# Performance work log

Measured on AMD Instinct MI355X. Metric: run time of the kernel, lower is better.

Reference implementation:

```python
import jax, jax.numpy as jnp
import numpy as np

B, T, E, H = 2, 4096, 1024, 16
D = E // H  # head dim = 64

def setup_inputs() -> dict:
    key = jax.random.key(0)
    ks = jax.random.split(key, 5)
    x = jax.random.normal(ks[0], (B, T, E), dtype=jnp.float32)
    # torch Linear(n_embed, 3*n_embed): y = x @ W.T + b ; we store W already transposed as (E, 3E)
    w_qkv = jax.random.normal(ks[1], (E, 3 * E), dtype=jnp.float32) * (1.0 / np.sqrt(E))
    b_qkv = jax.random.normal(ks[2], (3 * E,), dtype=jnp.float32) * 0.02
    w_out = jax.random.normal(ks[3], (E, E), dtype=jnp.float32) * (1.0 / np.sqrt(E))
    b_out = jax.random.normal(ks[4], (E,), dtype=jnp.float32) * 0.02
    return {"x": x, "w_qkv": w_qkv, "b_qkv": b_qkv, "w_out": w_out, "b_out": b_out}

def reference(x, w_qkv, b_qkv, w_out, b_out):
    b, t, e = x.shape
    qkv = x @ w_qkv + b_qkv                      # (B,T,3E)
    # matches torch: view(B,T,H,3D) then chunk(3, dim=-1)
    qkv = qkv.reshape(b, t, H, 3 * D)
    q, k, v = jnp.split(qkv, 3, axis=-1)          # each (B,T,H,D)
    q = q.transpose(0, 2, 1, 3)                   # (B,H,T,D)
    k = k.transpose(0, 2, 1, 3)
    v = v.transpose(0, 2, 1, 3)
    scores = jnp.einsum('bhqd,bhkd->bhqk', q, k) / jnp.sqrt(jnp.float32(D))
    causal = jnp.tril(jnp.ones((t, t), dtype=bool))
    scores = jnp.where(causal, scores, jnp.float32(-jnp.inf))
    w = jax.nn.softmax(scores, axis=-1)           # (B,H,T,T)
    out = jnp.einsum('bhqk,bhkd->bhqd', w, v)     # (B,H,T,D)
    out = out.transpose(0, 2, 1, 3).reshape(b, t, e)
    return out @ w_out + b_out
```

## Files before the change

### kernel.cpp

```cpp
#include <hip/hip_runtime.h>
#include <stdint.h>
#include <math.h>

#define T_SEQ 4096

typedef __attribute__((ext_vector_type(8))) short short8;
typedef __attribute__((ext_vector_type(4))) float f32x4;
typedef __attribute__((ext_vector_type(16))) float f32x16;
typedef __attribute__((ext_vector_type(4))) uint16_t u16x4;

__device__ __forceinline__ uint16_t f2bf(float f) {
  uint32_t u = __float_as_uint(f);
  u += 0x7FFFu + ((u >> 16) & 1u);
  return (uint16_t)(u >> 16);
}

__device__ __forceinline__ void gload_lds16(const uint16_t* g, uint16_t* l) {
  __builtin_amdgcn_global_load_lds(
      (const __attribute__((address_space(1))) void*)g,
      (__attribute__((address_space(3))) void*)l, 16, 0, 0);
}

__global__ void __launch_bounds__(256) k_cvt(const float* __restrict__ in,
                                             uint16_t* __restrict__ out, int n4) {
  int i = blockIdx.x * 256 + threadIdx.x;
  if (i >= n4) return;
  float4 v = reinterpret_cast<const float4*>(in)[i];
  u16x4 o = { f2bf(v.x), f2bf(v.y), f2bf(v.z), f2bf(v.w) };
  reinterpret_cast<u16x4*>(out)[i] = o;
}

__global__ void __launch_bounds__(256) k_tc(const float* __restrict__ w,
                                            uint16_t* __restrict__ wt, int R, int C) {
  __shared__ uint16_t tile[32][33];
  int tx = threadIdx.x & 31, ty = threadIdx.x >> 5;
  int r0 = blockIdx.y * 32, c0 = blockIdx.x * 32;
#pragma unroll
  for (int i = 0; i < 4; i++)
    tile[ty + 8 * i][tx] = f2bf(w[(size_t)(r0 + ty + 8 * i) * C + c0 + tx]);
  __syncthreads();
#pragma unroll
  for (int i = 0; i < 4; i++)
    wt[(size_t)(c0 + ty + 8 * i) * R + r0 + tx] = tile[tx][ty + 8 * i];
}

__global__ void __launch_bounds__(256) k_vt(const uint16_t* __restrict__ qkv,
                                            uint16_t* __restrict__ vT) {
  __shared__ uint16_t tile[64][65];
  const int bh = blockIdx.y, b = bh >> 4, h = bh & 15;
  const int t0 = blockIdx.x * 64;
  const int tid = threadIdx.x;
  const int r = tid >> 3, c8 = tid & 7;
  const uint16_t* src = qkv + ((size_t)b * T_SEQ + t0) * 3072 + h * 192 + 128;
#pragma unroll
  for (int i = 0; i < 2; i++) {
    int row = r + 32 * i;
    short8 v = *reinterpret_cast<const short8*>(src + (size_t)row * 3072 + c8 * 8);
#pragma unroll
    for (int j = 0; j < 8; j++) tile[row][c8 * 8 + j] = (uint16_t)v[j];
  }
  __syncthreads();
  uint16_t* dst = vT + ((size_t)bh * 64) * T_SEQ + t0;
#pragma unroll
  for (int i = 0; i < 2; i++) {
    int d = r + 32 * i;
    short8 v;
#pragma unroll
    for (int j = 0; j < 8; j++) v[j] = (short)tile[c8 * 8 + j][d];
    *reinterpret_cast<short8*>(dst + (size_t)d * T_SEQ + c8 * 8) = v;
  }
}

template <int BF16_OUT>
__global__ void __launch_bounds__(256, 2) k_gemm(const uint16_t* __restrict__ A,
                                                 const uint16_t* __restrict__ BT,
                                                 const float* __restrict__ bias,
                                                 void* __restrict__ Cout,
                                                 int M, int N, int K) {
  __shared__ __align__(16) uint16_t As[2][128 * 64];
  __shared__ __align__(16) uint16_t Bs[2][128 * 64];
  const int tid = threadIdx.x;
  const int lane = tid & 63, wid = tid >> 6;
  const int lr = lane & 15, lg = lane >> 4;
  const int wr = wid >> 1, wc = wid & 1;

  const int bid = blockIdx.x;
  const int cpx = gridDim.x >> 3;
  const int lin = (bid & 7) * cpx + (bid >> 3);
  const int mt = M >> 7;
  const int n0 = (lin / mt) * 128;
  const int m0 = (lin % mt) * 128;

  const f32x4 vzero = {0.f, 0.f, 0.f, 0.f};
  f32x4 acc[4][4];
#pragma unroll
  for (int i = 0; i < 4; i++)
#pragma unroll
    for (int j = 0; j < 4; j++) acc[i][j] = vzero;

  const int sl = lane >> 3, ss = lane & 7;
  const int swzs = (ss ^ sl) * 8;
  const uint16_t* a0 = A + (size_t)(m0 + wid * 32 + sl) * K + swzs;
  const uint16_t* b0 = BT + (size_t)(n0 + wid * 32 + sl) * K + swzs;
  const size_t r8 = (size_t)8 * K;

#define STAGE(bsel, t)                                                   \
  do {                                                                   \
    const int koff_ = (t) * 64;                                          \
    gload_lds16(a0 + koff_,          &As[bsel][(wid * 32 + 0) * 64]);    \
    gload_lds16(a0 + r8 + koff_,     &As[bsel][(wid * 32 + 8) * 64]);    \
    gload_lds16(a0 + 2 * r8 + koff_, &As[bsel][(wid * 32 + 16) * 64]);   \
    gload_lds16(a0 + 3 * r8 + koff_, &As[bsel][(wid * 32 + 24) * 64]);   \
    gload_lds16(b0 + koff_,          &Bs[bsel][(wid * 32 + 0) * 64]);    \
    gload_lds16(b0 + r8 + koff_,     &Bs[bsel][(wid * 32 + 8) * 64]);    \
    gload_lds16(b0 + 2 * r8 + koff_, &Bs[bsel][(wid * 32 + 16) * 64]);   \
    gload_lds16(b0 + 3 * r8 + koff_, &Bs[bsel][(wid * 32 + 24) * 64]);   \
  } while (0)

  const int nt = K >> 6;
  const int fsw = lr & 7;
  STAGE(0, 0);
  STAGE(1, 1);
  __syncthreads();

  for (int t = 0; t < nt; ++t) {
    const int cur = t & 1;
#pragma unroll
    for (int ks = 0; ks < 2; ++ks) {
      const int col = (((ks * 4 + lg) ^ fsw) * 8);
      short8 af[4], bf[4];
#pragma unroll
      for (int mi = 0; mi < 4; ++mi)
        af[mi] = *reinterpret_cast<const short8*>(
            &As[cur][(wr * 64 + mi * 16 + lr) * 64 + col]);
#pragma unroll
      for (int nj = 0; nj < 4; ++nj)
        bf[nj] = *reinterpret_cast<const short8*>(
            &Bs[cur][(wc * 64 + nj * 16 + lr) * 64 + col]);
      __builtin_amdgcn_s_setprio(1);
#pragma unroll
      for (int mi = 0; mi < 4; ++mi)
#pragma unroll
        for (int nj = 0; nj < 4; ++nj)
          acc[mi][nj] = __builtin_amdgcn_mfma_f32_16x16x32_bf16(af[mi], bf[nj], acc[mi][nj], 0, 0, 0);
      __builtin_amdgcn_s_setprio(0);
    }
    __syncthreads();
    if (t + 2 < nt) STAGE(cur, t + 2);
  }
#undef STAGE

#pragma unroll
  for (int nj = 0; nj < 4; nj++) {
    int col = n0 + wc * 64 + nj * 16 + lr;
    float bv = bias[col];
#pragma unroll
    for (int mi = 0; mi < 4; mi++) {
      int rowb = m0 + wr * 64 + mi * 16 + lg * 4;
#pragma unroll
      for (int r = 0; r < 4; r++) {
        float v = acc[mi][nj][r] + bv;
        if (BF16_OUT)
          ((uint16_t*)Cout)[(size_t)(rowb + r) * N + col] = f2bf(v);
        else
          ((float*)Cout)[(size_t)(rowb + r) * N + col] = v;
      }
    }
  }
}

#define KVB 64
__global__ void __launch_bounds__(256) k_attn(const uint16_t* __restrict__ qkv,
                                              const uint16_t* __restrict__ vT,
                                              uint16_t* __restrict__ out) {
  __shared__ __align__(16) char lds[32768];
  const int tid = threadIdx.x;
  const int lane = tid & 63, wid = tid >> 6;
  const int l31 = lane & 31, hi = lane >> 5;
  const int hi4 = hi * 4;

  const int bid = blockIdx.x;
  const int xcd = bid & 7, j = bid >> 3;
  const int bh = xcd * 4 + (j & 3);
  const int qt = 31 - (j >> 2);
  const int b = bh >> 4, h = bh & 15;
  const int q0 = qt * 128;
  const size_t rowbase = (size_t)b * T_SEQ;
  const int hoff = h * 192;
  const uint16_t* Kg = qkv + rowbase * 3072 + hoff + 64;
  const uint16_t* Vg = vT + (size_t)bh * 64 * T_SEQ;

  const int sr = tid >> 3, sc = tid & 7;
  const int wsw = (sc ^ (sr & 7)) * 16;
  const float C_SC = 0.180336881f;

  int rslot[4];
#pragma unroll
  for (int c = 0; c < 4; c++) rslot[c] = (((2 * c + hi) ^ (lane & 7)) << 4);
  const int rowb128 = l31 * 128;

  const int qrow = q0 + wid * 32 + l31;
  short8 qf[4];
#pragma unroll
  for (int ks = 0; ks < 4; ks++) {
    short8 raw = *reinterpret_cast<const short8*>(
        qkv + (rowbase + qrow) * 3072 + hoff + hi * 8 + ks * 16);
    union { short8 s; uint32_t u[4]; } pk;
#pragma unroll
    for (int e = 0; e < 4; e++) {
      float f0 = __uint_as_float(((uint32_t)(uint16_t)raw[2 * e]) << 16) * C_SC;
      float f1 = __uint_as_float(((uint32_t)(uint16_t)raw[2 * e + 1]) << 16) * C_SC;
      asm("v_cvt_pk_bf16_f32 %0, %1, %2" : "=v"(pk.u[e]) : "v"(f0), "v"(f1));
    }
    qf[ks] = pk.s;
  }

  f32x16 o0, o1, zero16;
#pragma unroll
  for (int i = 0; i < 16; i++) zero16[i] = 0.f;
  o0 = zero16; o1 = zero16;
  float lpart = 0.f;

  const int nkt = 2 * qt + 2;
  const int qwmax = q0 + wid * 32 + 31;

  short8 rk0, rk1, rv0, rv1;
  rk0 = *reinterpret_cast<const short8*>(Kg + (size_t)sr * 3072 + sc * 8);
  rk1 = *reinterpret_cast<const short8*>(Kg + (size_t)(sr + 32) * 3072 + sc * 8);
  rv0 = *reinterpret_cast<const short8*>(Vg + (size_t)sr * T_SEQ + sc * 8);
  rv1 = *reinterpret_cast<const short8*>(Vg + (size_t)(sr + 32) * T_SEQ + sc * 8);
  {
    char* kb0 = lds;
    char* vb0 = lds + 16384;
    *reinterpret_cast<short8*>(kb0 + sr * 128 + wsw) = rk0;
    *reinterpret_cast<short8*>(kb0 + (sr + 32) * 128 + wsw) = rk1;
    *reinterpret_cast<short8*>(vb0 + sr * 128 + wsw) = rv0;
    *reinterpret_cast<short8*>(vb0 + (sr + 32) * 128 + wsw) = rv1;
  }
  if (nkt > 1) {
    rk0 = *reinterpret_cast<const short8*>(Kg + (size_t)(KVB + sr) * 3072 + sc * 8);
    rk1 = *reinterpret_cast<const short8*>(Kg + (size_t)(KVB + sr + 32) * 3072 + sc * 8);
    rv0 = *reinterpret_cast<const short8*>(Vg + (size_t)sr * T_SEQ + KVB + sc * 8);
    rv1 = *reinterpret_cast<const short8*>(Vg + (size_t)(sr + 32) * T_SEQ + KVB + sc * 8);
  }

  for (int kt = 0; kt < nkt; kt++) {
    __syncthreads();
    if (kt + 1 < nkt) {
      const int nsel = (kt + 1) & 1;
      char* kb = lds + (nsel ? 8192 : 0);
      char* vb = lds + 16384 + (nsel ? 8192 : 0);
      *reinterpret_cast<short8*>(kb + sr * 128 + wsw) = rk0;
      *reinterpret_cast<short8*>(kb + (sr + 32) * 128 + wsw) = rk1;
      *reinterpret_cast<short8*>(vb + sr * 128 + wsw) = rv0;
      *reinterpret_cast<short8*>(vb + (sr + 32) * 128 + wsw) = rv1;
      if (kt + 2 < nkt) {
        int k0n = (kt + 2) * KVB;
        rk0 = *reinterpret_cast<const short8*>(Kg + (size_t)(k0n + sr) * 3072 + sc * 8);
        rk1 = *reinterpret_cast<const short8*>(Kg + (size_t)(k0n + sr + 32) * 3072 + sc * 8);
        rv0 = *reinterpret_cast<const short8*>(Vg + (size_t)sr * T_SEQ + k0n + sc * 8);
        rv1 = *reinterpret_cast<const short8*>(Vg + (size_t)(sr + 32) * T_SEQ + k0n + sc * 8);
      }
    }

    if (kt * KVB <= qwmax) {
      const int csel = kt & 1;
      char* kcur = lds + (csel ? 8192 : 0);
      char* vcur = lds + 16384 + (csel ? 8192 : 0);
      const int ktb = kt * KVB;
      const bool notfull = (ktb + 63 > q0 + wid * 32);

      f32x16 s0 = zero16, s1 = zero16;
      __builtin_amdgcn_s_setprio(1);
#pragma unroll
      for (int ks = 0; ks < 4; ks++) {
        short8 kf0 = *reinterpret_cast<const short8*>(kcur + rowb128 + rslot[ks]);
        short8 kf1 = *reinterpret_cast<const short8*>(kcur + 4096 + rowb128 + rslot[ks]);
        s0 = __builtin_amdgcn_mfma_f32_32x32x16_bf16(kf0, qf[ks], s0, 0, 0, 0);
        s1 = __builtin_amdgcn_mfma_f32_32x32x16_bf16(kf1, qf[ks], s1, 0, 0, 0);
      }
      __builtin_amdgcn_s_setprio(0);

      uint32_t u0[8], u1[8];
#define SMAX_KB(SV, KB, U)                                                    \
  do {                                                                        \
    _Pragma("unroll")                                                         \
    for (int r = 0; r < 16; r++) {                                            \
      float v = SV[r];                                                        \
      if (notfull) {                                                          \
        int key = ktb + (KB) * 32 + (r & 3) + 8 * (r >> 2) + hi4;             \
        if (key > qrow) v = -INFINITY;                                        \
      }                                                                       \
      float p = __builtin_amdgcn_exp2f(v);                                    \
      SV[r] = p;                                                              \
      lpart += p;                                                             \
    }                                                                         \
    _Pragma("unroll")                                                         \
    for (int jj = 0; jj < 8; jj++)                                            \
      asm("v_cvt_pk_bf16_f32 %0, %1, %2"                                      \
          : "=v"(U[jj]) : "v"(SV[2 * jj]), "v"(SV[2 * jj + 1]));              \
    asm volatile("v_permlane32_swap_b32 %0, %1" : "+v"(U[0]), "+v"(U[2]));    \
    asm volatile("v_permlane32_swap_b32 %0, %1" : "+v"(U[1]), "+v"(U[3]));    \
    asm volatile("v_permlane32_swap_b32 %0, %1" : "+v"(U[4]), "+v"(U[6]));    \
    asm volatile("v_permlane32_swap_b32 %0, %1" : "+v"(U[5]), "+v"(U[7]));    \
  } while (0)

      SMAX_KB(s0, 0, u0);
      SMAX_KB(s1, 1, u1);
#undef SMAX_KB

      union { uint32_t u[4]; short8 s; } pf;
      __builtin_amdgcn_s_setprio(1);
#pragma unroll
      for (int kv = 0; kv < 4; kv++) {
        if (kv == 0) { pf.u[0] = u0[0]; pf.u[1] = u0[1]; pf.u[2] = u0[2]; pf.u[3] = u0[3]; }
        else if (kv == 1) { pf.u[0] = u0[4]; pf.u[1] = u0[5]; pf.u[2] = u0[6]; pf.u[3] = u0[7]; }
        else if (kv == 2) { pf.u[0] = u1[0]; pf.u[1] = u1[1]; pf.u[2] = u1[2]; pf.u[3] = u1[3]; }
        else { pf.u[0] = u1[4]; pf.u[1] = u1[5]; pf.u[2] = u1[6]; pf.u[3] = u1[7]; }
        short8 vf0 = *reinterpret_cast<const short8*>(vcur + rowb128 + rslot[kv]);
        short8 vf1 = *reinterpret_cast<const short8*>(vcur + 4096 + rowb128 + rslot[kv]);
        o0 = __builtin_amdgcn_mfma_f32_32x32x16_bf16(vf0, pf.s, o0, 0, 0, 0);
        o1 = __builtin_amdgcn_mfma_f32_32x32x16_bf16(vf1, pf.s, o1, 0, 0, 0);
      }
      __builtin_amdgcn_s_setprio(0);
    }
  }

  __syncthreads();
  float ltot = lpart + __shfl_xor(lpart, 32);
  float inv = 1.0f / ltot;
  char* scrb = lds + wid * 8192;
#pragma unroll
  for (int g = 0; g < 4; g++) {
    f32x4 w0, w1;
#pragma unroll
    for (int e = 0; e < 4; e++) { w0[e] = o0[4 * g + e] * inv; w1[e] = o1[4 * g + e] * inv; }
    int s0i = 2 * g + hi, s1i = s0i + 8;
    *reinterpret_cast<f32x4*>(scrb + l31 * 256 + ((s0i ^ (l31 & 7)) << 4)) = w0;
    *reinterpret_cast<f32x4*>(scrb + l31 * 256 + ((s1i ^ (l31 & 7)) << 4)) = w1;
  }
  asm volatile("s_waitcnt lgkmcnt(0)" ::: "memory");
  __builtin_amdgcn_sched_barrier(0);
  {
    int row = lane >> 1, half = lane & 1;
    uint16_t tmp[32];
#pragma unroll
    for (int k = 0; k < 8; k++) {
      f32x4 vv = *reinterpret_cast<const f32x4*>(
          scrb + row * 256 + (((half * 8 + k) ^ (row & 7)) << 4));
#pragma unroll
      for (int e = 0; e < 4; e++) tmp[k * 4 + e] = f2bf(vv[e]);
    }
    uint16_t* op = out + (rowbase + q0 + wid * 32 + row) * 1024 + h * 64 + half * 32;
#pragma unroll
    for (int k = 0; k < 4; k++)
      *reinterpret_cast<short8*>(op + k * 8) = *reinterpret_cast<const short8*>(tmp + k * 8);
  }
}

extern "C" void kernel_launch(void* const* d_in, const int* in_sizes, int n_in,
                              void* d_out, int out_size, void* d_ws, size_t ws_size,
                              hipStream_t stream) {
  const float* x = (const float*)d_in[0];
  const float* w_qkv = (const float*)d_in[1];
  const float* b_qkv = (const float*)d_in[2];
  const float* w_out = (const float*)d_in[3];
  const float* b_out = (const float*)d_in[4];
  float* out = (float*)d_out;

  uint8_t* ws = (uint8_t*)d_ws;
  uint16_t* x_bf  = (uint16_t*)(ws);
  uint16_t* wqkvT = (uint16_t*)(ws + (16u << 20));
  uint16_t* woutT = (uint16_t*)(ws + (22u << 20));
  uint16_t* qkv   = (uint16_t*)(ws + (24u << 20));
  uint16_t* vTbuf = (uint16_t*)(ws + (72u << 20));
  uint16_t* attn_o = x_bf;

  k_cvt<<<8192, 256, 0, stream>>>(x, x_bf, 2097152);
  k_tc<<<dim3(96, 32), 256, 0, stream>>>(w_qkv, wqkvT, 1024, 3072);
  k_tc<<<dim3(32, 32), 256, 0, stream>>>(w_out, woutT, 1024, 1024);
  k_gemm<1><<<1536, 256, 0, stream>>>(x_bf, wqkvT, b_qkv, qkv, 8192, 3072, 1024);
  k_vt<<<dim3(64, 32), 256, 0, stream>>>(qkv, vTbuf);
  k_attn<<<1024, 256, 0, stream>>>(qkv, vTbuf, attn_o);
  k_gemm<0><<<512, 256, 0, stream>>>(attn_o, woutT, b_out, out, 8192, 1024, 1024);
}
```

Baseline: 228.2 us.

## Use 256x256-tile GEMM with 512 threads for QKV projection

Adds a new GEMM kernel with 256x256 output tiles, 8 waves, and double-buffered LDS loads via global_load_lds, and uses it for the QKV projection instead of the 128x128-tile kernel. Larger tiles raise arithmetic intensity and cut redundant global loads of A and B. In exchange each thread holds 128 accumulator floats, which raises register pressure. The grid also shrinks to 384 blocks, so fewer blocks are available to fill the compute units.

```diff
diff --git a/kernel.cpp b/kernel.cpp
--- a/kernel.cpp
+++ b/kernel.cpp
@@ -165,6 +165,90 @@
         else
           ((float*)Cout)[(size_t)(rowb + r) * N + col] = v;
       }
+    }
+  }
+}
+
+__global__ void __launch_bounds__(512, 2) k_gemm256(const uint16_t* __restrict__ A,
+                                                    const uint16_t* __restrict__ BT,
+                                                    const float* __restrict__ bias,
+                                                    uint16_t* __restrict__ Cout,
+                                                    int M, int N, int K) {
+  __shared__ __align__(16) uint16_t As[2][256 * 32];
+  __shared__ __align__(16) uint16_t Bs[2][256 * 32];
+  const int tid = threadIdx.x;
+  const int lane = tid & 63, wid = tid >> 6;
+  const int lr = lane & 15, lg = lane >> 4;
+  const int wr = wid >> 2, wc = wid & 3;
+
+  const int bid = blockIdx.x;
+  const int cpx = gridDim.x >> 3;
+  const int lin = (bid & 7) * cpx + (bid >> 3);
+  const int mt = M >> 8;
+  const int n0 = (lin / mt) * 256;
+  const int m0 = (lin % mt) * 256;
+
+  const f32x4 vzero = {0.f, 0.f, 0.f, 0.f};
+  f32x4 acc[8][4];
+#pragma unroll
+  for (int i = 0; i < 8; i++)
+#pragma unroll
+    for (int j = 0; j < 4; j++) acc[i][j] = vzero;
+
+  const int row0 = tid >> 2;
+  const int gc = (tid & 3) ^ ((tid >> 3) & 3);
+  const uint16_t* a0 = A + (size_t)(m0 + row0) * K + gc * 8;
+  const uint16_t* b0 = BT + (size_t)(n0 + row0) * K + gc * 8;
+  const size_t rstep = (size_t)128 * K;
+
+#define STAGE2(bsel, t)                                                    \
+  do {                                                                     \
+    const int ko_ = (t) * 32;                                              \
+    gload_lds16(a0 + ko_,         &As[bsel][wid * 512]);                   \
+    gload_lds16(a0 + rstep + ko_, &As[bsel][wid * 512 + 4096]);            \
+    gload_lds16(b0 + ko_,         &Bs[bsel][wid * 512]);                   \
+    gload_lds16(b0 + rstep + ko_, &Bs[bsel][wid * 512 + 4096]);            \
+  } while (0)
+
+  const int nt = K >> 5;
+  const int fc = (lg ^ ((lr >> 1) & 3)) * 8;
+  STAGE2(0, 0);
+  STAGE2(1, 1);
+  __syncthreads();
+
+  for (int t = 0; t < nt; ++t) {
+    const int cur = t & 1;
+    short8 af[8], bf[4];
+#pragma unroll
+    for (int mi = 0; mi < 8; ++mi)
+      af[mi] = *reinterpret_cast<const short8*>(
+          &As[cur][(wr * 128 + mi * 16 + lr) * 32 + fc]);
+#pragma unroll
+    for (int nj = 0; nj < 4; ++nj)
+      bf[nj] = *reinterpret_cast<const short8*>(
+          &Bs[cur][(wc * 64 + nj * 16 + lr) * 32 + fc]);
+    __builtin_amdgcn_s_setprio(1);
+#pragma unroll
+    for (int mi = 0; mi < 8; ++mi)
+#pragma unroll
+      for (int nj = 0; nj < 4; ++nj)
+        acc[mi][nj] = __builtin_amdgcn_mfma_f32_16x16x32_bf16(af[mi], bf[nj], acc[mi][nj], 0, 0, 0);
+    __builtin_amdgcn_s_setprio(0);
+    __syncthreads();
+    if (t + 2 < nt) STAGE2(cur, t + 2);
+  }
+#undef STAGE2
+
+#pragma unroll
+  for (int nj = 0; nj < 4; nj++) {
+    int col = n0 + wc * 64 + nj * 16 + lr;
+    float bv = bias[col];
+#pragma unroll
+    for (int mi = 0; mi < 8; mi++) {
+      int rowb = m0 + wr * 128 + mi * 16 + lg * 4;
+#pragma unroll
+      for (int r = 0; r < 4; r++)
+        Cout[(size_t)(rowb + r) * N + col] = f2bf(acc[mi][nj][r] + bv);
     }
   }
 }
@@ -379,7 +463,7 @@
   k_cvt<<<8192, 256, 0, stream>>>(x, x_bf, 2097152);
   k_tc<<<dim3(96, 32), 256, 0, stream>>>(w_qkv, wqkvT, 1024, 3072);
   k_tc<<<dim3(32, 32), 256, 0, stream>>>(w_out, woutT, 1024, 1024);
-  k_gemm<1><<<1536, 256, 0, stream>>>(x_bf, wqkvT, b_qkv, qkv, 8192, 3072, 1024);
+  k_gemm256<<<384, 512, 0, stream>>>(x_bf, wqkvT, b_qkv, qkv, 8192, 3072, 1024);
   k_vt<<<dim3(64, 32), 256, 0, stream>>>(qkv, vTbuf);
   k_attn<<<1024, 256, 0, stream>>>(qkv, vTbuf, attn_o);
   k_gemm<0><<<512, 256, 0, stream>>>(attn_o, woutT, b_out, out, 8192, 1024, 1024);
```

Result: slower. 242.7 us (+6.4%).
